# Optimization experiments

Hardware: AMD Instinct MI355X
Metric: run time of the kernel (lower is better)

The kernel has to match this reference:

```python
import jax, jax.numpy as jnp
import numpy as np

NUM_USERS = 100000
NUM_ITEMS = 100000
N = NUM_USERS + NUM_ITEMS
D = 64
E = 1200000


def setup_inputs() -> dict:
    key = jax.random.key(0)
    k1, k2, k3, k4, k5 = jax.random.split(key, 5)
    edge_index = jax.random.randint(k1, (2, E), 0, N, dtype=jnp.int64)
    user_emb = jax.random.normal(k2, (NUM_USERS, D), dtype=jnp.float32)
    item_emb = jax.random.normal(k3, (NUM_ITEMS, D), dtype=jnp.float32)
    W1 = jax.random.normal(k4, (D, D), dtype=jnp.float32) / np.sqrt(D)
    b1 = jnp.zeros((D,), dtype=jnp.float32)
    W2 = jax.random.normal(k5, (D, D), dtype=jnp.float32) / np.sqrt(D)
    b2 = jnp.zeros((D,), dtype=jnp.float32)
    return {"edge_index": edge_index, "user_emb": user_emb, "item_emb": item_emb,
            "W1": W1, "b1": b1, "W2": W2, "b2": b2}


def _gcn_conv(x, row, col, norm, W, b, n_nodes):
    # x: [N, D]; row/col: [E+N] (with self-loops); norm: [E+N]
    x = x @ W                                  # linear transform (no bias in lin)
    msg = x[row] * norm[:, None]               # gather + scale (memory-bound)
    out = jax.ops.segment_sum(msg, col, num_segments=n_nodes)  # scatter-add
    return out + b


def reference(edge_index, user_emb, item_emb, W1, b1, W2, b2):
    x = jnp.concatenate([user_emb, item_emb], axis=0)  # [N, D]
    n_nodes = x.shape[0]
    # gcn_norm: add self-loops, symmetric deg^{-1/2} normalization
    sl = jnp.arange(n_nodes, dtype=edge_index.dtype)
    row = jnp.concatenate([edge_index[0], sl])
    col = jnp.concatenate([edge_index[1], sl])
    deg = jax.ops.segment_sum(jnp.ones_like(col, dtype=x.dtype), col,
                              num_segments=n_nodes)
    dinv = jnp.where(deg > 0, jax.lax.rsqrt(jnp.maximum(deg, 1e-12)), 0.0)
    norm = dinv[row] * dinv[col]
    x = _gcn_conv(x, row, col, norm, W1, b1, n_nodes)
    x = _gcn_conv(x, row, col, norm, W2, b2, n_nodes)
    return x
```

## Files before the change

kernel.cpp:

```cpp
#include <hip/hip_runtime.h>

#define DIM 64
#define GPW 4
#define BSHIFT 9
#define BSPAN 512
#define MAXNB 512

typedef __attribute__((ext_vector_type(8))) __bf16 bf16x8;
typedef __attribute__((ext_vector_type(4))) __bf16 bf16x4;
typedef __attribute__((ext_vector_type(8))) unsigned short u16x8;
typedef __attribute__((ext_vector_type(4))) float f32x4;

__device__ __forceinline__ f32x4 mfma16(bf16x8 a, bf16x8 b, f32x4 c) {
    return __builtin_amdgcn_mfma_f32_16x16x32_bf16(a, b, c, 0, 0, 0);
}

__device__ __forceinline__ float bf2f(unsigned short u) {
    return __uint_as_float((unsigned)u << 16);
}


__global__ void zerob_kernel(int* __restrict__ b) { b[threadIdx.x] = 0; }

__global__ __launch_bounds__(512) void bucket_count_kernel(
    const int* __restrict__ ei, int* __restrict__ bcnt, int E_, int NB) {
    __shared__ int hist[MAXNB];
    int tid = threadIdx.x;
    for (int i = tid; i < NB; i += 512) hist[i] = 0;
    __syncthreads();
    int chunk = (E_ + gridDim.x - 1) / gridDim.x;
    int e0 = blockIdx.x * chunk, e1 = min(E_, e0 + chunk);
    for (int e = e0 + tid; e < e1; e += 512)
        atomicAdd(&hist[ei[E_ + e] >> BSHIFT], 1);
    __syncthreads();
    for (int i = tid; i < NB; i += 512)
        if (hist[i]) atomicAdd(&bcnt[i], hist[i]);
}

__global__ __launch_bounds__(512) void bucket_scan_kernel(
    const int* __restrict__ bcnt, int* __restrict__ bptr, int* __restrict__ bcur,
    int* __restrict__ rowptr, int NB, int N_, int E_) {
    __shared__ int sm[512];
    int tid = threadIdx.x;
    int v = (tid < NB) ? bcnt[tid] : 0;
    sm[tid] = v;
    __syncthreads();
    for (int off = 1; off < 512; off <<= 1) {
        int t = 0;
        if (tid >= off) t = sm[tid - off];
        __syncthreads();
        if (tid >= off) sm[tid] += t;
        __syncthreads();
    }
    if (tid < NB) {
        int ex = sm[tid] - v;
        bptr[tid] = ex;
        bcur[tid] = ex;
    }
    if (tid == 0) { bptr[NB] = E_; rowptr[N_] = E_; }
}

__global__ __launch_bounds__(512) void scatter_kernel(
    const int* __restrict__ ei, int* __restrict__ bcur,
    unsigned* __restrict__ packed, int E_, int NB) {
    __shared__ int h[MAXNB];
    int tid = threadIdx.x;
    int chunk = (E_ + gridDim.x - 1) / gridDim.x;
    int e0 = blockIdx.x * chunk, e1 = min(E_, e0 + chunk);
    for (int i = tid; i < NB; i += 512) h[i] = 0;
    __syncthreads();
    for (int e = e0 + tid; e < e1; e += 512)
        atomicAdd(&h[ei[E_ + e] >> BSHIFT], 1);
    __syncthreads();
    for (int i = tid; i < NB; i += 512) {
        int c = h[i];
        h[i] = c ? atomicAdd(&bcur[i], c) : 0;
    }
    __syncthreads();
    for (int e = e0 + tid; e < e1; e += 512) {
        int s = ei[e], d = ei[E_ + e];
        int b = d >> BSHIFT;
        int pos = atomicAdd(&h[b], 1);
        packed[pos] = ((unsigned)s << BSHIFT) | (unsigned)(d & (BSPAN - 1));
    }
}

__global__ __launch_bounds__(256) void bucket_sort_kernel(
    const unsigned* __restrict__ packed, const int* __restrict__ bptr,
    int* __restrict__ rowptr, int* __restrict__ srcs,
    float* __restrict__ dinv, int N_) {
    __shared__ int cnt[BSPAN];
    __shared__ int sc[256];
    int tid = threadIdx.x;
    int b = blockIdx.x;
    int beg = bptr[b], end = bptr[b + 1];
    int node0 = b << BSHIFT;
    int nn = min(BSPAN, N_ - node0);
    cnt[tid] = 0; cnt[tid + 256] = 0;
    __syncthreads();
    for (int i = beg + tid; i < end; i += 256)
        atomicAdd(&cnt[packed[i] & (BSPAN - 1)], 1);
    __syncthreads();
    int degA = cnt[tid], degB = cnt[tid + 256];
    int a0 = cnt[2 * tid], a1 = cnt[2 * tid + 1];
    if (tid < nn) dinv[node0 + tid] = rsqrtf((float)(1 + degA));
    if (tid + 256 < nn) dinv[node0 + tid + 256] = rsqrtf((float)(1 + degB));
    int tot = a0 + a1;
    sc[tid] = tot;
    __syncthreads();
    for (int off = 1; off < 256; off <<= 1) {
        int t = 0;
        if (tid >= off) t = sc[tid - off];
        __syncthreads();
        if (tid >= off) sc[tid] += t;
        __syncthreads();
    }
    int ex = sc[tid] - tot;
    cnt[2 * tid] = ex;
    cnt[2 * tid + 1] = ex + a0;
    __syncthreads();
    if (tid < nn) rowptr[node0 + tid] = beg + cnt[tid];
    if (tid + 256 < nn) rowptr[node0 + tid + 256] = beg + cnt[tid + 256];
    __syncthreads();
    for (int i = beg + tid; i < end; i += 256) {
        unsigned p = packed[i];
        int pos = atomicAdd(&cnt[p & (BSPAN - 1)], 1);
        srcs[beg + pos] = (int)(p >> BSHIFT);
    }
}


template <bool BF16IN>
__global__ __launch_bounds__(256) void gemm_kernel(
    const void* __restrict__ xa_, const void* __restrict__ xb_, int split,
    const float* __restrict__ W, const float* __restrict__ dinv,
    __bf16* __restrict__ h, int n, int ngroups) {
    int lane = threadIdx.x & 63;
    int q = lane >> 4, t = lane & 15;
    int wv = __builtin_amdgcn_readfirstlane(threadIdx.x >> 6);
    int g0 = (blockIdx.x * 4 + wv) * GPW;
    if (g0 >= ngroups) return;

    bf16x8 Bf[4][2];
#pragma unroll
    for (int nt = 0; nt < 4; ++nt)
#pragma unroll
        for (int kt = 0; kt < 2; ++kt) {
            bf16x8 f;
#pragma unroll
            for (int j = 0; j < 8; ++j)
                f[j] = (__bf16)W[(kt * 32 + q * 8 + j) * DIM + nt * 16 + t];
            Bf[nt][kt] = f;
        }

    auto loadA = [&](int r0, f32x4* raw) {
        int row = r0 + t;
        if (row >= n) row = n - 1;
        if constexpr (BF16IN) {
            const __bf16* xr = (const __bf16*)xa_ + (size_t)row * DIM;
            raw[0] = *(const f32x4*)(xr + q * 8);
            raw[1] = *(const f32x4*)(xr + 32 + q * 8);
        } else {
            const float* xr = (row < split)
                ? ((const float*)xa_ + (size_t)row * DIM)
                : ((const float*)xb_ + (size_t)(row - split) * DIM);
            raw[0] = *(const f32x4*)(xr + q * 8);
            raw[1] = *(const f32x4*)(xr + q * 8 + 4);
            raw[2] = *(const f32x4*)(xr + 32 + q * 8);
            raw[3] = *(const f32x4*)(xr + 32 + q * 8 + 4);
        }
    };

    f32x4 cur[4];
    loadA(g0 * 16, cur);

#pragma unroll 1
    for (int gi = 0; gi < GPW; ++gi) {
        int g = g0 + gi;
        if (g >= ngroups) break;
        int r0 = g * 16;
        f32x4 nxt[4];
        bool pf = (gi + 1 < GPW) && (g + 1 < ngroups);
        if (pf) loadA(r0 + 16, nxt);

        bf16x8 A0, A1;
        if constexpr (BF16IN) {
            A0 = __builtin_bit_cast(bf16x8, cur[0]);
            A1 = __builtin_bit_cast(bf16x8, cur[1]);
        } else {
#pragma unroll
            for (int j = 0; j < 4; ++j) {
                A0[j] = (__bf16)cur[0][j]; A0[j + 4] = (__bf16)cur[1][j];
                A1[j] = (__bf16)cur[2][j]; A1[j + 4] = (__bf16)cur[3][j];
            }
        }

        f32x4 z = {0.f, 0.f, 0.f, 0.f};
        f32x4 acc[4];
#pragma unroll
        for (int nt = 0; nt < 4; ++nt)
            acc[nt] = mfma16(A1, Bf[nt][1], mfma16(A0, Bf[nt][0], z));

        f32x4 d4 = *(const f32x4*)(dinv + r0 + q * 4);
#pragma unroll
        for (int nt = 0; nt < 4; ++nt)
#pragma unroll
            for (int reg = 0; reg < 4; ++reg) {
                int row = r0 + q * 4 + reg;
                if (row < n)
                    h[(size_t)row * DIM + nt * 16 + t] =
                        (__bf16)(acc[nt][reg] * d4[reg]);
            }
#pragma unroll
        for (int i = 0; i < 4; ++i) cur[i] = nxt[i];
    }
}

template <typename OutT>
__global__ __launch_bounds__(256) void agg_kernel(
    const int* __restrict__ rowptr, const int* __restrict__ srcs,
    const __bf16* __restrict__ h, const float* __restrict__ bias,
    const float* __restrict__ dinv, OutT* __restrict__ out, int n) {
    int lane = threadIdx.x & 63;
    int t8 = lane & 7;
    int wv = threadIdx.x >> 6;
    int node = (blockIdx.x * 4 + wv) * 8 + (lane >> 3);
    bool alive = node < n;
    int nd = alive ? node : (n - 1);
    int beg = rowptr[nd], end = rowptr[nd + 1];

    u16x8 sv = *(const u16x8*)(h + (size_t)nd * DIM + t8 * 8);
    float acc[8];
#pragma unroll
    for (int j = 0; j < 8; ++j) acc[j] = bf2f(sv[j]);

    int i = beg;
    while (i < end) {
        int idx = i + t8;
        int sl = (idx < end) ? srcs[idx] : 0;
        u16x8 vv[8];
#pragma unroll
        for (int k = 0; k < 8; ++k) {
            int s = __shfl(sl, (lane & 56) | k);
            vv[k] = *(const u16x8*)(h + (size_t)s * DIM + t8 * 8);
        }
#pragma unroll
        for (int k = 0; k < 8; ++k)
            if (i + k < end) {
#pragma unroll
                for (int j = 0; j < 8; ++j) acc[j] += bf2f(vv[k][j]);
            }
        i += 8;
    }

    float dn = dinv[nd];
    f32x4 b0 = *(const f32x4*)(bias + t8 * 8);
    f32x4 b1 = *(const f32x4*)(bias + t8 * 8 + 4);
    float r[8];
#pragma unroll
    for (int j = 0; j < 4; ++j) {
        r[j]     = fmaf(dn, acc[j],     b0[j]);
        r[j + 4] = fmaf(dn, acc[j + 4], b1[j]);
    }
    if (alive) {
        if constexpr (sizeof(OutT) == 4) {
            f32x4 o0 = {r[0], r[1], r[2], r[3]};
            f32x4 o1 = {r[4], r[5], r[6], r[7]};
            float* op = (float*)out + (size_t)node * DIM + t8 * 8;
            *(f32x4*)op = o0;
            *(f32x4*)(op + 4) = o1;
        } else {
            bf16x8 o;
#pragma unroll
            for (int j = 0; j < 8; ++j) o[j] = (__bf16)r[j];
            *(bf16x8*)((__bf16*)out + (size_t)node * DIM + t8 * 8) = o;
        }
    }
}

static inline size_t align16(size_t x) { return (x + 15) & ~(size_t)15; }

extern "C" void kernel_launch(void* const* d_in, const int* in_sizes, int n_in,
                              void* d_out, int out_size, void* d_ws, size_t ws_size,
                              hipStream_t stream) {
    const int* ei         = (const int*)d_in[0];
    const float* user_emb = (const float*)d_in[1];
    const float* item_emb = (const float*)d_in[2];
    const float* W1 = (const float*)d_in[3];
    const float* b1 = (const float*)d_in[4];
    const float* W2 = (const float*)d_in[5];
    const float* b2 = (const float*)d_in[6];
    float* out = (float*)d_out;

    const int E_ = in_sizes[0] / 2;
    const int NU = in_sizes[1] / DIM;
    const int NI = in_sizes[2] / DIM;
    const int N_ = NU + NI;
    const int NB = (N_ + BSPAN - 1) >> BSHIFT;

    char* p = (char*)d_ws;
    int* srcs   = (int*)p;               p += align16((size_t)E_ * 4);
    __bf16* h   = (__bf16*)p;            p += align16((size_t)N_ * DIM * 2);
    __bf16* t1  = (__bf16*)p;            p += align16((size_t)N_ * DIM * 2);
    float* dinv = (float*)p;             p += align16((size_t)N_ * 4);
    int* rowptr = (int*)p;               p += align16((size_t)(N_ + 1) * 4);
    int* bcnt   = (int*)p;               p += align16((size_t)MAXNB * 4);
    int* bptr   = (int*)p;               p += align16((size_t)(MAXNB + 1) * 4);
    int* bcur   = (int*)p;               p += align16((size_t)MAXNB * 4);
    unsigned* packed = (unsigned*)t1;

    zerob_kernel<<<1, MAXNB, 0, stream>>>(bcnt);
    bucket_count_kernel<<<256, 512, 0, stream>>>(ei, bcnt, E_, NB);
    bucket_scan_kernel<<<1, 512, 0, stream>>>(bcnt, bptr, bcur, rowptr, NB, N_, E_);
    scatter_kernel<<<256, 512, 0, stream>>>(ei, bcur, packed, E_, NB);
    bucket_sort_kernel<<<NB, 256, 0, stream>>>(packed, bptr, rowptr, srcs, dinv, N_);

    int NG = (N_ + 15) / 16;
    int gblocks = (NG + 4 * GPW - 1) / (4 * GPW);
    int ablocks = (N_ + 31) / 32;

    gemm_kernel<false><<<gblocks, 256, 0, stream>>>(user_emb, item_emb, NU,
                                                    W1, dinv, h, N_, NG);
    agg_kernel<__bf16><<<ablocks, 256, 0, stream>>>(rowptr, srcs, h, b1, dinv, t1, N_);
    gemm_kernel<true><<<gblocks, 256, 0, stream>>>(t1, t1, N_,
                                                   W2, dinv, h, N_, NG);
    agg_kernel<float><<<ablocks, 256, 0, stream>>>(rowptr, srcs, h, b2, dinv, out, N_);
}
```

Measured before the change: 255.0 us.

## Fuse layer-1 aggregation with layer-2 GEMM via shared-memory tile

```diff
diff --git a/kernel.cpp b/kernel.cpp
--- a/kernel.cpp
+++ b/kernel.cpp
@@ -130,9 +130,8 @@
 }
 
 
-template <bool BF16IN>
 __global__ __launch_bounds__(256) void gemm_kernel(
-    const void* __restrict__ xa_, const void* __restrict__ xb_, int split,
+    const float* __restrict__ xa_, const float* __restrict__ xb_, int split,
     const float* __restrict__ W, const float* __restrict__ dinv,
     __bf16* __restrict__ h, int n, int ngroups) {
     int lane = threadIdx.x & 63;
@@ -156,19 +155,13 @@
     auto loadA = [&](int r0, f32x4* raw) {
         int row = r0 + t;
         if (row >= n) row = n - 1;
-        if constexpr (BF16IN) {
-            const __bf16* xr = (const __bf16*)xa_ + (size_t)row * DIM;
-            raw[0] = *(const f32x4*)(xr + q * 8);
-            raw[1] = *(const f32x4*)(xr + 32 + q * 8);
-        } else {
-            const float* xr = (row < split)
-                ? ((const float*)xa_ + (size_t)row * DIM)
-                : ((const float*)xb_ + (size_t)(row - split) * DIM);
-            raw[0] = *(const f32x4*)(xr + q * 8);
-            raw[1] = *(const f32x4*)(xr + q * 8 + 4);
-            raw[2] = *(const f32x4*)(xr + 32 + q * 8);
-            raw[3] = *(const f32x4*)(xr + 32 + q * 8 + 4);
-        }
+        const float* xr = (row < split)
+            ? (xa_ + (size_t)row * DIM)
+            : (xb_ + (size_t)(row - split) * DIM);
+        raw[0] = __builtin_nontemporal_load((const f32x4*)(xr + q * 8));
+        raw[1] = __builtin_nontemporal_load((const f32x4*)(xr + q * 8 + 4));
+        raw[2] = __builtin_nontemporal_load((const f32x4*)(xr + 32 + q * 8));
+        raw[3] = __builtin_nontemporal_load((const f32x4*)(xr + 32 + q * 8 + 4));
     };
 
     f32x4 cur[4];
@@ -184,15 +177,10 @@
         if (pf) loadA(r0 + 16, nxt);
 
         bf16x8 A0, A1;
-        if constexpr (BF16IN) {
-            A0 = __builtin_bit_cast(bf16x8, cur[0]);
-            A1 = __builtin_bit_cast(bf16x8, cur[1]);
-        } else {
-#pragma unroll
-            for (int j = 0; j < 4; ++j) {
-                A0[j] = (__bf16)cur[0][j]; A0[j + 4] = (__bf16)cur[1][j];
-                A1[j] = (__bf16)cur[2][j]; A1[j + 4] = (__bf16)cur[3][j];
-            }
+#pragma unroll
+        for (int j = 0; j < 4; ++j) {
+            A0[j] = (__bf16)cur[0][j]; A0[j + 4] = (__bf16)cur[1][j];
+            A1[j] = (__bf16)cur[2][j]; A1[j + 4] = (__bf16)cur[3][j];
         }
 
         f32x4 z = {0.f, 0.f, 0.f, 0.f};
@@ -216,11 +204,98 @@
     }
 }
 
-template <typename OutT>
+__global__ __launch_bounds__(256) void agg_gemm_kernel(
+    const int* __restrict__ rowptr, const int* __restrict__ srcs,
+    const __bf16* __restrict__ h, const float* __restrict__ b1,
+    const float* __restrict__ W2, const float* __restrict__ dinv,
+    __bf16* __restrict__ h2, int n) {
+    __shared__ __bf16 rows[32][72];
+    int lane = threadIdx.x & 63;
+    int t8 = lane & 7;
+    int wv = __builtin_amdgcn_readfirstlane(threadIdx.x >> 6);
+    int q = lane >> 4, t = lane & 15;
+    int lrow = wv * 8 + (lane >> 3);
+    int node = blockIdx.x * 32 + lrow;
+    int nd = (node < n) ? node : (n - 1);
+
+    bf16x8 Bf[4][2];
+    if (wv < 2) {
+#pragma unroll
+        for (int nt = 0; nt < 4; ++nt)
+#pragma unroll
+            for (int kt = 0; kt < 2; ++kt) {
+                bf16x8 f;
+#pragma unroll
+                for (int j = 0; j < 8; ++j)
+                    f[j] = (__bf16)W2[(kt * 32 + q * 8 + j) * DIM + nt * 16 + t];
+                Bf[nt][kt] = f;
+            }
+    }
+
+    int beg = rowptr[nd], end = rowptr[nd + 1];
+    u16x8 sv = *(const u16x8*)(h + (size_t)nd * DIM + t8 * 8);
+    float acc[8];
+#pragma unroll
+    for (int j = 0; j < 8; ++j) acc[j] = bf2f(sv[j]);
+
+    int i = beg;
+    while (i < end) {
+        int idx = i + t8;
+        int sl = (idx < end) ? srcs[idx] : 0;
+        u16x8 vv[8];
+#pragma unroll
+        for (int k = 0; k < 8; ++k) {
+            int s = __shfl(sl, (lane & 56) | k);
+            vv[k] = *(const u16x8*)(h + (size_t)s * DIM + t8 * 8);
+        }
+#pragma unroll
+        for (int k = 0; k < 8; ++k)
+            if (i + k < end) {
+#pragma unroll
+                for (int j = 0; j < 8; ++j) acc[j] += bf2f(vv[k][j]);
+            }
+        i += 8;
+    }
+
+    float dn = dinv[nd];
+    f32x4 b0 = *(const f32x4*)(b1 + t8 * 8);
+    f32x4 b1v = *(const f32x4*)(b1 + t8 * 8 + 4);
+    bf16x8 o;
+#pragma unroll
+    for (int j = 0; j < 4; ++j) {
+        o[j]     = (__bf16)fmaf(dn, acc[j],     b0[j]);
+        o[j + 4] = (__bf16)fmaf(dn, acc[j + 4], b1v[j]);
+    }
+    *(bf16x8*)&rows[lrow][t8 * 8] = o;
+    __syncthreads();
+
+    if (wv < 2) {
+        const __bf16* ap = &rows[wv * 16 + t][0];
+        bf16x8 A0 = *(const bf16x8*)(ap + q * 8);
+        bf16x8 A1 = *(const bf16x8*)(ap + 32 + q * 8);
+        f32x4 z = {0.f, 0.f, 0.f, 0.f};
+        f32x4 acc2[4];
+#pragma unroll
+        for (int nt = 0; nt < 4; ++nt)
+            acc2[nt] = mfma16(A1, Bf[nt][1], mfma16(A0, Bf[nt][0], z));
+        int gr0 = blockIdx.x * 32 + wv * 16;
+        f32x4 d4 = *(const f32x4*)(dinv + gr0 + q * 4);
+#pragma unroll
+        for (int nt = 0; nt < 4; ++nt)
+#pragma unroll
+            for (int reg = 0; reg < 4; ++reg) {
+                int row = gr0 + q * 4 + reg;
+                if (row < n)
+                    h2[(size_t)row * DIM + nt * 16 + t] =
+                        (__bf16)(acc2[nt][reg] * d4[reg]);
+            }
+    }
+}
+
 __global__ __launch_bounds__(256) void agg_kernel(
     const int* __restrict__ rowptr, const int* __restrict__ srcs,
     const __bf16* __restrict__ h, const float* __restrict__ bias,
-    const float* __restrict__ dinv, OutT* __restrict__ out, int n) {
+    const float* __restrict__ dinv, float* __restrict__ out, int n) {
     int lane = threadIdx.x & 63;
     int t8 = lane & 7;
     int wv = threadIdx.x >> 6;
@@ -256,25 +331,16 @@
     float dn = dinv[nd];
     f32x4 b0 = *(const f32x4*)(bias + t8 * 8);
     f32x4 b1 = *(const f32x4*)(bias + t8 * 8 + 4);
-    float r[8];
-#pragma unroll
-    for (int j = 0; j < 4; ++j) {
-        r[j]     = fmaf(dn, acc[j],     b0[j]);
-        r[j + 4] = fmaf(dn, acc[j + 4], b1[j]);
-    }
     if (alive) {
-        if constexpr (sizeof(OutT) == 4) {
-            f32x4 o0 = {r[0], r[1], r[2], r[3]};
-            f32x4 o1 = {r[4], r[5], r[6], r[7]};
-            float* op = (float*)out + (size_t)node * DIM + t8 * 8;
-            *(f32x4*)op = o0;
-            *(f32x4*)(op + 4) = o1;
-        } else {
-            bf16x8 o;
-#pragma unroll
-            for (int j = 0; j < 8; ++j) o[j] = (__bf16)r[j];
-            *(bf16x8*)((__bf16*)out + (size_t)node * DIM + t8 * 8) = o;
-        }
+        f32x4 o0, o1;
+#pragma unroll
+        for (int j = 0; j < 4; ++j) {
+            o0[j] = fmaf(dn, acc[j],     b0[j]);
+            o1[j] = fmaf(dn, acc[j + 4], b1[j]);
+        }
+        float* op = out + (size_t)node * DIM + t8 * 8;
+        __builtin_nontemporal_store(o0, (f32x4*)op);
+        __builtin_nontemporal_store(o1, (f32x4*)(op + 4));
     }
 }
 
@@ -319,10 +385,9 @@
     int gblocks = (NG + 4 * GPW - 1) / (4 * GPW);
     int ablocks = (N_ + 31) / 32;
 
-    gemm_kernel<false><<<gblocks, 256, 0, stream>>>(user_emb, item_emb, NU,
-                                                    W1, dinv, h, N_, NG);
-    agg_kernel<__bf16><<<ablocks, 256, 0, stream>>>(rowptr, srcs, h, b1, dinv, t1, N_);
-    gemm_kernel<true><<<gblocks, 256, 0, stream>>>(t1, t1, N_,
-                                                   W2, dinv, h, N_, NG);
-    agg_kernel<float><<<ablocks, 256, 0, stream>>>(rowptr, srcs, h, b2, dinv, out, N_);
-}
+    gemm_kernel<<<gblocks, 256, 0, stream>>>(user_emb, item_emb, NU,
+                                             W1, dinv, h, N_, NG);
+    agg_gemm_kernel<<<ablocks, 256, 0, stream>>>(rowptr, srcs, h, b1, W2,
+                                                 dinv, t1, N_);
+    agg_kernel<<<ablocks, 256, 0, stream>>>(rowptr, srcs, t1, b2, dinv, out, N_);
+}
```

Measured after the change: 261.4 us. 1.03x slower.

## Fuse CSR build into one cooperative kernel with grid syncs

Applied to the files above, without the earlier changes.

```diff
diff --git a/kernel.cpp b/kernel.cpp
--- a/kernel.cpp
+++ b/kernel.cpp
@@ -1,4 +1,7 @@
 #include <hip/hip_runtime.h>
+#include <hip/hip_cooperative_groups.h>
+
+namespace cg = cooperative_groups;
 
 #define DIM 64
 #define GPW 4
@@ -19,113 +22,100 @@
     return __uint_as_float((unsigned)u << 16);
 }
 
-
-__global__ void zerob_kernel(int* __restrict__ b) { b[threadIdx.x] = 0; }
-
-__global__ __launch_bounds__(512) void bucket_count_kernel(
-    const int* __restrict__ ei, int* __restrict__ bcnt, int E_, int NB) {
+__global__ __launch_bounds__(512) void csr_build_kernel(
+    const int* __restrict__ ei, unsigned* __restrict__ packed,
+    int* __restrict__ bcnt, int* __restrict__ bcur0,
+    int* __restrict__ rowptr, int* __restrict__ srcs,
+    float* __restrict__ dinv, int E_, int N_, int NB) {
+    cg::grid_group grid = cg::this_grid();
     __shared__ int hist[MAXNB];
+    __shared__ int sm[512];
     int tid = threadIdx.x;
+    int bid = blockIdx.x;
+    int nblk = gridDim.x;
+
+    if (bid == 0) {
+        bcnt[tid] = 0;
+        bcur0[tid] = 0;
+        if (tid == 0) rowptr[N_] = E_;
+    }
+    grid.sync();
+
     for (int i = tid; i < NB; i += 512) hist[i] = 0;
     __syncthreads();
-    int chunk = (E_ + gridDim.x - 1) / gridDim.x;
-    int e0 = blockIdx.x * chunk, e1 = min(E_, e0 + chunk);
+    int chunk = (E_ + nblk - 1) / nblk;
+    int e0 = bid * chunk, e1 = min(E_, e0 + chunk);
     for (int e = e0 + tid; e < e1; e += 512)
         atomicAdd(&hist[ei[E_ + e] >> BSHIFT], 1);
     __syncthreads();
     for (int i = tid; i < NB; i += 512)
         if (hist[i]) atomicAdd(&bcnt[i], hist[i]);
-}
-
-__global__ __launch_bounds__(512) void bucket_scan_kernel(
-    const int* __restrict__ bcnt, int* __restrict__ bptr, int* __restrict__ bcur,
-    int* __restrict__ rowptr, int NB, int N_, int E_) {
-    __shared__ int sm[512];
-    int tid = threadIdx.x;
-    int v = (tid < NB) ? bcnt[tid] : 0;
-    sm[tid] = v;
-    __syncthreads();
-    for (int off = 1; off < 512; off <<= 1) {
-        int t = 0;
-        if (tid >= off) t = sm[tid - off];
-        __syncthreads();
-        if (tid >= off) sm[tid] += t;
-        __syncthreads();
-    }
-    if (tid < NB) {
-        int ex = sm[tid] - v;
-        bptr[tid] = ex;
-        bcur[tid] = ex;
-    }
-    if (tid == 0) { bptr[NB] = E_; rowptr[N_] = E_; }
-}
-
-__global__ __launch_bounds__(512) void scatter_kernel(
-    const int* __restrict__ ei, int* __restrict__ bcur,
-    unsigned* __restrict__ packed, int E_, int NB) {
-    __shared__ int h[MAXNB];
-    int tid = threadIdx.x;
-    int chunk = (E_ + gridDim.x - 1) / gridDim.x;
-    int e0 = blockIdx.x * chunk, e1 = min(E_, e0 + chunk);
-    for (int i = tid; i < NB; i += 512) h[i] = 0;
+    grid.sync();
+
+    {
+        int v = (tid < NB) ? bcnt[tid] : 0;
+        sm[tid] = v;
+        __syncthreads();
+        for (int off = 1; off < 512; off <<= 1) {
+            int t = 0;
+            if (tid >= off) t = sm[tid - off];
+            __syncthreads();
+            if (tid >= off) sm[tid] += t;
+            __syncthreads();
+        }
+        hist[tid] = sm[tid] - v;
+    }
+    __syncthreads();
+
+    for (int i = tid; i < NB; i += 512) sm[i] = 0;
     __syncthreads();
     for (int e = e0 + tid; e < e1; e += 512)
-        atomicAdd(&h[ei[E_ + e] >> BSHIFT], 1);
+        atomicAdd(&sm[ei[E_ + e] >> BSHIFT], 1);
     __syncthreads();
     for (int i = tid; i < NB; i += 512) {
-        int c = h[i];
-        h[i] = c ? atomicAdd(&bcur[i], c) : 0;
+        int c = sm[i];
+        sm[i] = c ? (hist[i] + atomicAdd(&bcur0[i], c)) : 0;
     }
     __syncthreads();
     for (int e = e0 + tid; e < e1; e += 512) {
         int s = ei[e], d = ei[E_ + e];
         int b = d >> BSHIFT;
-        int pos = atomicAdd(&h[b], 1);
+        int pos = atomicAdd(&sm[b], 1);
         packed[pos] = ((unsigned)s << BSHIFT) | (unsigned)(d & (BSPAN - 1));
     }
-}
-
-__global__ __launch_bounds__(256) void bucket_sort_kernel(
-    const unsigned* __restrict__ packed, const int* __restrict__ bptr,
-    int* __restrict__ rowptr, int* __restrict__ srcs,
-    float* __restrict__ dinv, int N_) {
-    __shared__ int cnt[BSPAN];
-    __shared__ int sc[256];
-    int tid = threadIdx.x;
-    int b = blockIdx.x;
-    int beg = bptr[b], end = bptr[b + 1];
-    int node0 = b << BSHIFT;
-    int nn = min(BSPAN, N_ - node0);
-    cnt[tid] = 0; cnt[tid + 256] = 0;
-    __syncthreads();
-    for (int i = beg + tid; i < end; i += 256)
-        atomicAdd(&cnt[packed[i] & (BSPAN - 1)], 1);
-    __syncthreads();
-    int degA = cnt[tid], degB = cnt[tid + 256];
-    int a0 = cnt[2 * tid], a1 = cnt[2 * tid + 1];
-    if (tid < nn) dinv[node0 + tid] = rsqrtf((float)(1 + degA));
-    if (tid + 256 < nn) dinv[node0 + tid + 256] = rsqrtf((float)(1 + degB));
-    int tot = a0 + a1;
-    sc[tid] = tot;
-    __syncthreads();
-    for (int off = 1; off < 256; off <<= 1) {
-        int t = 0;
-        if (tid >= off) t = sc[tid - off];
-        __syncthreads();
-        if (tid >= off) sc[tid] += t;
-        __syncthreads();
-    }
-    int ex = sc[tid] - tot;
-    cnt[2 * tid] = ex;
-    cnt[2 * tid + 1] = ex + a0;
-    __syncthreads();
-    if (tid < nn) rowptr[node0 + tid] = beg + cnt[tid];
-    if (tid + 256 < nn) rowptr[node0 + tid + 256] = beg + cnt[tid + 256];
-    __syncthreads();
-    for (int i = beg + tid; i < end; i += 256) {
-        unsigned p = packed[i];
-        int pos = atomicAdd(&cnt[p & (BSPAN - 1)], 1);
-        srcs[beg + pos] = (int)(p >> BSHIFT);
+    grid.sync();
+
+    for (int b = bid; b < NB; b += nblk) {
+        int beg = hist[b];
+        int end2 = (b + 1 < MAXNB) ? hist[b + 1] : E_;
+        if (b + 1 == NB) end2 = E_;
+        int node0 = b << BSHIFT;
+        int nn = min(BSPAN, N_ - node0);
+        sm[tid] = 0;
+        __syncthreads();
+        for (int i = beg + tid; i < end2; i += 512)
+            atomicAdd(&sm[packed[i] & (BSPAN - 1)], 1);
+        __syncthreads();
+        int deg = sm[tid];
+        if (tid < nn) dinv[node0 + tid] = rsqrtf((float)(1 + deg));
+        for (int off = 1; off < 512; off <<= 1) {
+            int t = 0;
+            if (tid >= off) t = sm[tid - off];
+            __syncthreads();
+            if (tid >= off) sm[tid] += t;
+            __syncthreads();
+        }
+        int ex = sm[tid] - deg;
+        if (tid < nn) rowptr[node0 + tid] = beg + ex;
+        __syncthreads();
+        sm[tid] = ex;
+        __syncthreads();
+        for (int i = beg + tid; i < end2; i += 512) {
+            unsigned p = packed[i];
+            int pos = atomicAdd(&sm[p & (BSPAN - 1)], 1);
+            srcs[beg + pos] = (int)(p >> BSHIFT);
+        }
+        __syncthreads();
     }
 }
 
@@ -164,10 +154,10 @@
             const float* xr = (row < split)
                 ? ((const float*)xa_ + (size_t)row * DIM)
                 : ((const float*)xb_ + (size_t)(row - split) * DIM);
-            raw[0] = *(const f32x4*)(xr + q * 8);
-            raw[1] = *(const f32x4*)(xr + q * 8 + 4);
-            raw[2] = *(const f32x4*)(xr + 32 + q * 8);
-            raw[3] = *(const f32x4*)(xr + 32 + q * 8 + 4);
+            raw[0] = __builtin_nontemporal_load((const f32x4*)(xr + q * 8));
+            raw[1] = __builtin_nontemporal_load((const f32x4*)(xr + q * 8 + 4));
+            raw[2] = __builtin_nontemporal_load((const f32x4*)(xr + 32 + q * 8));
+            raw[3] = __builtin_nontemporal_load((const f32x4*)(xr + 32 + q * 8 + 4));
         }
     };
 
@@ -256,23 +246,24 @@
     float dn = dinv[nd];
     f32x4 b0 = *(const f32x4*)(bias + t8 * 8);
     f32x4 b1 = *(const f32x4*)(bias + t8 * 8 + 4);
-    float r[8];
-#pragma unroll
-    for (int j = 0; j < 4; ++j) {
-        r[j]     = fmaf(dn, acc[j],     b0[j]);
-        r[j + 4] = fmaf(dn, acc[j + 4], b1[j]);
-    }
     if (alive) {
         if constexpr (sizeof(OutT) == 4) {
-            f32x4 o0 = {r[0], r[1], r[2], r[3]};
-            f32x4 o1 = {r[4], r[5], r[6], r[7]};
+            f32x4 o0, o1;
+#pragma unroll
+            for (int j = 0; j < 4; ++j) {
+                o0[j] = fmaf(dn, acc[j],     b0[j]);
+                o1[j] = fmaf(dn, acc[j + 4], b1[j]);
+            }
             float* op = (float*)out + (size_t)node * DIM + t8 * 8;
-            *(f32x4*)op = o0;
-            *(f32x4*)(op + 4) = o1;
+            __builtin_nontemporal_store(o0, (f32x4*)op);
+            __builtin_nontemporal_store(o1, (f32x4*)(op + 4));
         } else {
             bf16x8 o;
 #pragma unroll
-            for (int j = 0; j < 8; ++j) o[j] = (__bf16)r[j];
+            for (int j = 0; j < 4; ++j) {
+                o[j]     = (__bf16)fmaf(dn, acc[j],     b0[j]);
+                o[j + 4] = (__bf16)fmaf(dn, acc[j + 4], b1[j]);
+            }
             *(bf16x8*)((__bf16*)out + (size_t)node * DIM + t8 * 8) = o;
         }
     }
@@ -305,15 +296,18 @@
     float* dinv = (float*)p;             p += align16((size_t)N_ * 4);
     int* rowptr = (int*)p;               p += align16((size_t)(N_ + 1) * 4);
     int* bcnt   = (int*)p;               p += align16((size_t)MAXNB * 4);
-    int* bptr   = (int*)p;               p += align16((size_t)(MAXNB + 1) * 4);
-    int* bcur   = (int*)p;               p += align16((size_t)MAXNB * 4);
+    int* bcur0  = (int*)p;               p += align16((size_t)MAXNB * 4);
     unsigned* packed = (unsigned*)t1;
 
-    zerob_kernel<<<1, MAXNB, 0, stream>>>(bcnt);
-    bucket_count_kernel<<<256, 512, 0, stream>>>(ei, bcnt, E_, NB);
-    bucket_scan_kernel<<<1, 512, 0, stream>>>(bcnt, bptr, bcur, rowptr, NB, N_, E_);
-    scatter_kernel<<<256, 512, 0, stream>>>(ei, bcur, packed, E_, NB);
-    bucket_sort_kernel<<<NB, 256, 0, stream>>>(packed, bptr, rowptr, srcs, dinv, N_);
+    {
+        void* args[] = {
+            (void*)&ei, (void*)&packed, (void*)&bcnt, (void*)&bcur0,
+            (void*)&rowptr, (void*)&srcs, (void*)&dinv,
+            (void*)&E_, (void*)&N_, (void*)&NB,
+        };
+        hipLaunchCooperativeKernel((const void*)csr_build_kernel,
+                                   dim3((unsigned)NB), dim3(512), args, 0, stream);
+    }
 
     int NG = (N_ + 15) / 16;
     int gblocks = (NG + 4 * GPW - 1) / (4 * GPW);
```

Measured after the change: 397.7 us. 56.0% more time.

## Fuse CSR bucket count, scan and scatter into one cooperative kernel

Applied to the files above, without the earlier changes.

```diff
diff --git a/kernel.cpp b/kernel.cpp
--- a/kernel.cpp
+++ b/kernel.cpp
@@ -5,9 +5,9 @@
 #define BSHIFT 9
 #define BSPAN 512
 #define MAXNB 512
+#define CSRB 512
 
 typedef __attribute__((ext_vector_type(8))) __bf16 bf16x8;
-typedef __attribute__((ext_vector_type(4))) __bf16 bf16x4;
 typedef __attribute__((ext_vector_type(8))) unsigned short u16x8;
 typedef __attribute__((ext_vector_type(4))) float f32x4;
 
@@ -19,30 +19,37 @@
     return __uint_as_float((unsigned)u << 16);
 }
 
-
-__global__ void zerob_kernel(int* __restrict__ b) { b[threadIdx.x] = 0; }
-
-__global__ __launch_bounds__(512) void bucket_count_kernel(
-    const int* __restrict__ ei, int* __restrict__ bcnt, int E_, int NB) {
+__global__ __launch_bounds__(512) void csr_count_scatter_kernel(
+    const int* __restrict__ ei, unsigned* __restrict__ packed,
+    int* __restrict__ bcnt, int* __restrict__ bcur0, int* __restrict__ bar,
+    int* __restrict__ bptr, int* __restrict__ rowptr,
+    int E_, int N_, int nblk) {
     __shared__ int hist[MAXNB];
+    __shared__ int sm[512];
     int tid = threadIdx.x;
-    for (int i = tid; i < NB; i += 512) hist[i] = 0;
-    __syncthreads();
-    int chunk = (E_ + gridDim.x - 1) / gridDim.x;
-    int e0 = blockIdx.x * chunk, e1 = min(E_, e0 + chunk);
+    int bid = blockIdx.x;
+    int chunk = (E_ + nblk - 1) / nblk;
+    int e0 = bid * chunk, e1 = min(E_, e0 + chunk);
+
+    hist[tid] = 0;
+    __syncthreads();
     for (int e = e0 + tid; e < e1; e += 512)
         atomicAdd(&hist[ei[E_ + e] >> BSHIFT], 1);
     __syncthreads();
-    for (int i = tid; i < NB; i += 512)
-        if (hist[i]) atomicAdd(&bcnt[i], hist[i]);
-}
-
-__global__ __launch_bounds__(512) void bucket_scan_kernel(
-    const int* __restrict__ bcnt, int* __restrict__ bptr, int* __restrict__ bcur,
-    int* __restrict__ rowptr, int NB, int N_, int E_) {
-    __shared__ int sm[512];
-    int tid = threadIdx.x;
-    int v = (tid < NB) ? bcnt[tid] : 0;
+    if (hist[tid]) atomicAdd(&bcnt[tid], hist[tid]);
+
+    __syncthreads();
+    if (tid == 0) {
+        __hip_atomic_fetch_add(bar, 1, __ATOMIC_RELEASE,
+                               __HIP_MEMORY_SCOPE_AGENT);
+        while (__hip_atomic_load(bar, __ATOMIC_ACQUIRE,
+                                 __HIP_MEMORY_SCOPE_AGENT) < nblk)
+            __builtin_amdgcn_s_sleep(2);
+    }
+    __syncthreads();
+
+    int v = __hip_atomic_load(&bcnt[tid], __ATOMIC_RELAXED,
+                              __HIP_MEMORY_SCOPE_AGENT);
     sm[tid] = v;
     __syncthreads();
     for (int off = 1; off < 512; off <<= 1) {
@@ -52,35 +59,27 @@
         if (tid >= off) sm[tid] += t;
         __syncthreads();
     }
-    if (tid < NB) {
-        int ex = sm[tid] - v;
+    int ex = sm[tid] - v;
+    __syncthreads();
+    hist[tid] = ex;
+    if (bid == 0) {
         bptr[tid] = ex;
-        bcur[tid] = ex;
-    }
-    if (tid == 0) { bptr[NB] = E_; rowptr[N_] = E_; }
-}
-
-__global__ __launch_bounds__(512) void scatter_kernel(
-    const int* __restrict__ ei, int* __restrict__ bcur,
-    unsigned* __restrict__ packed, int E_, int NB) {
-    __shared__ int h[MAXNB];
-    int tid = threadIdx.x;
-    int chunk = (E_ + gridDim.x - 1) / gridDim.x;
-    int e0 = blockIdx.x * chunk, e1 = min(E_, e0 + chunk);
-    for (int i = tid; i < NB; i += 512) h[i] = 0;
+        if (tid == 0) { bptr[512] = E_; rowptr[N_] = E_; }
+    }
+    __syncthreads();
+
+    sm[tid] = 0;
     __syncthreads();
     for (int e = e0 + tid; e < e1; e += 512)
-        atomicAdd(&h[ei[E_ + e] >> BSHIFT], 1);
-    __syncthreads();
-    for (int i = tid; i < NB; i += 512) {
-        int c = h[i];
-        h[i] = c ? atomicAdd(&bcur[i], c) : 0;
-    }
+        atomicAdd(&sm[ei[E_ + e] >> BSHIFT], 1);
+    __syncthreads();
+    int c = sm[tid];
+    sm[tid] = c ? (hist[tid] + atomicAdd(&bcur0[tid], c)) : 0;
     __syncthreads();
     for (int e = e0 + tid; e < e1; e += 512) {
         int s = ei[e], d = ei[E_ + e];
         int b = d >> BSHIFT;
-        int pos = atomicAdd(&h[b], 1);
+        int pos = atomicAdd(&sm[b], 1);
         packed[pos] = ((unsigned)s << BSHIFT) | (unsigned)(d & (BSPAN - 1));
     }
 }
@@ -164,10 +163,10 @@
             const float* xr = (row < split)
                 ? ((const float*)xa_ + (size_t)row * DIM)
                 : ((const float*)xb_ + (size_t)(row - split) * DIM);
-            raw[0] = *(const f32x4*)(xr + q * 8);
-            raw[1] = *(const f32x4*)(xr + q * 8 + 4);
-            raw[2] = *(const f32x4*)(xr + 32 + q * 8);
-            raw[3] = *(const f32x4*)(xr + 32 + q * 8 + 4);
+            raw[0] = __builtin_nontemporal_load((const f32x4*)(xr + q * 8));
+            raw[1] = __builtin_nontemporal_load((const f32x4*)(xr + q * 8 + 4));
+            raw[2] = __builtin_nontemporal_load((const f32x4*)(xr + 32 + q * 8));
+            raw[3] = __builtin_nontemporal_load((const f32x4*)(xr + 32 + q * 8 + 4));
         }
     };
 
@@ -256,23 +255,24 @@
     float dn = dinv[nd];
     f32x4 b0 = *(const f32x4*)(bias + t8 * 8);
     f32x4 b1 = *(const f32x4*)(bias + t8 * 8 + 4);
-    float r[8];
-#pragma unroll
-    for (int j = 0; j < 4; ++j) {
-        r[j]     = fmaf(dn, acc[j],     b0[j]);
-        r[j + 4] = fmaf(dn, acc[j + 4], b1[j]);
-    }
     if (alive) {
         if constexpr (sizeof(OutT) == 4) {
-            f32x4 o0 = {r[0], r[1], r[2], r[3]};
-            f32x4 o1 = {r[4], r[5], r[6], r[7]};
+            f32x4 o0, o1;
+#pragma unroll
+            for (int j = 0; j < 4; ++j) {
+                o0[j] = fmaf(dn, acc[j],     b0[j]);
+                o1[j] = fmaf(dn, acc[j + 4], b1[j]);
+            }
             float* op = (float*)out + (size_t)node * DIM + t8 * 8;
-            *(f32x4*)op = o0;
-            *(f32x4*)(op + 4) = o1;
+            __builtin_nontemporal_store(o0, (f32x4*)op);
+            __builtin_nontemporal_store(o1, (f32x4*)(op + 4));
         } else {
             bf16x8 o;
 #pragma unroll
-            for (int j = 0; j < 8; ++j) o[j] = (__bf16)r[j];
+            for (int j = 0; j < 4; ++j) {
+                o[j]     = (__bf16)fmaf(dn, acc[j],     b0[j]);
+                o[j + 4] = (__bf16)fmaf(dn, acc[j + 4], b1[j]);
+            }
             *(bf16x8*)((__bf16*)out + (size_t)node * DIM + t8 * 8) = o;
         }
     }
@@ -304,15 +304,24 @@
     __bf16* t1  = (__bf16*)p;            p += align16((size_t)N_ * DIM * 2);
     float* dinv = (float*)p;             p += align16((size_t)N_ * 4);
     int* rowptr = (int*)p;               p += align16((size_t)(N_ + 1) * 4);
+    int* bptr   = (int*)p;               p += align16((size_t)(MAXNB + 1) * 4);
     int* bcnt   = (int*)p;               p += align16((size_t)MAXNB * 4);
-    int* bptr   = (int*)p;               p += align16((size_t)(MAXNB + 1) * 4);
-    int* bcur   = (int*)p;               p += align16((size_t)MAXNB * 4);
+    int* bcur0  = (int*)p;               p += align16((size_t)MAXNB * 4);
+    int* bar    = (int*)p;               p += align16(16);
     unsigned* packed = (unsigned*)t1;
 
-    zerob_kernel<<<1, MAXNB, 0, stream>>>(bcnt);
-    bucket_count_kernel<<<256, 512, 0, stream>>>(ei, bcnt, E_, NB);
-    bucket_scan_kernel<<<1, 512, 0, stream>>>(bcnt, bptr, bcur, rowptr, NB, N_, E_);
-    scatter_kernel<<<256, 512, 0, stream>>>(ei, bcur, packed, E_, NB);
+    hipMemsetAsync(bcnt, 0, (size_t)MAXNB * 4 * 2 + 16, stream);
+
+    {
+        int nblk = CSRB;
+        void* args[] = {
+            (void*)&ei, (void*)&packed, (void*)&bcnt, (void*)&bcur0,
+            (void*)&bar, (void*)&bptr, (void*)&rowptr,
+            (void*)&E_, (void*)&N_, (void*)&nblk,
+        };
+        hipLaunchCooperativeKernel((const void*)csr_count_scatter_kernel,
+                                   dim3(CSRB), dim3(512), args, 0, stream);
+    }
     bucket_sort_kernel<<<NB, 256, 0, stream>>>(packed, bptr, rowptr, srcs, dinv, N_);
 
     int NG = (N_ + 15) / 16;
```

Result: slower. 328.0 us (+28.6%).
